# Kernel tuning notes

Measured on AMD Instinct MI355X. Metric: run time of the kernel, lower is better.

The kernel has to match this reference:

```python
import jax, jax.numpy as jnp
import numpy as np

N = 8192       # nodes
NFEAT = 512    # input features
NHID = 64      # per-head hidden
NHEADS = 4
NCLASS = 40
ALPHA = 0.2    # leaky_relu negative slope
EDGE_P = 0.01  # adjacency density (plus self-loops)


def setup_inputs() -> dict:
    key = jax.random.key(0)
    k = jax.random.split(key, 6)
    x = jax.random.normal(k[0], (N, NFEAT), dtype=jnp.float32)
    adj = jax.random.bernoulli(k[1], EDGE_P, (N, N))
    adj = adj | jnp.eye(N, dtype=bool)  # self-loops so no row is fully masked
    W1 = jax.random.normal(k[2], (NHEADS, NFEAT, NHID), dtype=jnp.float32) * 0.05
    a1 = jax.random.normal(k[3], (NHEADS, 2 * NHID), dtype=jnp.float32) * 0.05
    Wo = jax.random.normal(k[4], (NHEADS * NHID, NCLASS), dtype=jnp.float32) * 0.05
    ao = jax.random.normal(k[5], (2 * NCLASS,), dtype=jnp.float32) * 0.05
    return {"x": x, "adj": adj, "W1": W1, "a1": a1, "Wo": Wo, "ao": ao}


def _gat_head(h, adj, W, a, concat):
    # GAT attention head: e_ij = leaky_relu(a1 . Wh_i + a2 . Wh_j), masked by adj
    Wh = h @ W                      # [N, F']
    Fp = W.shape[1]
    f_src = Wh @ a[:Fp]             # [N]
    f_dst = Wh @ a[Fp:]             # [N]
    e = jax.nn.leaky_relu(f_src[:, None] + f_dst[None, :], negative_slope=ALPHA)
    e = jnp.where(adj, e, jnp.float32(-9e15))
    att = jax.nn.softmax(e, axis=1)  # [N, N]
    out = att @ Wh                   # [N, F']
    return jax.nn.elu(out) if concat else out


def reference(x, adj, W1, a1, Wo, ao):
    # dropout is identity in eval mode
    heads = [_gat_head(x, adj, W1[i], a1[i], concat=True) for i in range(NHEADS)]
    x1 = jnp.concatenate(heads, axis=1)            # [N, NHEADS*NHID]
    out = jax.nn.elu(_gat_head(x1, adj, Wo, ao, concat=False))  # [N, NCLASS]
    return jax.nn.log_softmax(out, axis=1)
```

## Files before the change

kernel.cpp:

```cpp
#include <hip/hip_runtime.h>
#include <hip/hip_bf16.h>


#define N_NODES 8192
#define STRIDE  192

typedef _Float16 f16x8 __attribute__((ext_vector_type(8)));
typedef float    f32x4 __attribute__((ext_vector_type(4)));

__global__ __launch_bounds__(256) void prep_k(
    const float* __restrict__ x, const unsigned char* __restrict__ adjb,
    const float* __restrict__ W1, const float* __restrict__ Wo,
    _Float16* __restrict__ xh, _Float16* __restrict__ B1t, _Float16* __restrict__ B2t,
    int* __restrict__ nbr, int* __restrict__ deg)
{
    const int b = blockIdx.x;
    const int tid = threadIdx.x;
    if (b < N_NODES) {
        __shared__ int cnt;
        if (tid == 0) cnt = 0;
        __syncthreads();
        const bool bytewise = (adjb[8193] == 1);
        if (bytewise) {
            const uint4* p = (const uint4*)(adjb + (size_t)b * N_NODES);
            #pragma unroll
            for (int q = 0; q < 2; ++q) {
                const int idx = tid + 256 * q;
                uint4 v = p[idx];
                unsigned int ws_[4] = {v.x, v.y, v.z, v.w};
                #pragma unroll
                for (int wj = 0; wj < 4; ++wj) {
                    unsigned int u = ws_[wj];
                    if (u) {
                        #pragma unroll
                        for (int by = 0; by < 4; ++by) {
                            if ((u >> (8 * by)) & 0xFFu) {
                                int c = idx * 16 + wj * 4 + by;
                                int pos = atomicAdd(&cnt, 1);
                                if (pos < STRIDE) nbr[(size_t)b * STRIDE + pos] = c;
                            }
                        }
                    }
                }
            }
        } else {
            const int4* p = (const int4*)((const int*)(const void*)adjb + (size_t)b * N_NODES);
            #pragma unroll
            for (int q = 0; q < 8; ++q) {
                const int idx = tid + 256 * q;
                int4 v = p[idx];
                if (v.x) { int pos = atomicAdd(&cnt, 1); if (pos < STRIDE) nbr[(size_t)b * STRIDE + pos] = idx * 4 + 0; }
                if (v.y) { int pos = atomicAdd(&cnt, 1); if (pos < STRIDE) nbr[(size_t)b * STRIDE + pos] = idx * 4 + 1; }
                if (v.z) { int pos = atomicAdd(&cnt, 1); if (pos < STRIDE) nbr[(size_t)b * STRIDE + pos] = idx * 4 + 2; }
                if (v.w) { int pos = atomicAdd(&cnt, 1); if (pos < STRIDE) nbr[(size_t)b * STRIDE + pos] = idx * 4 + 3; }
            }
        }
        __syncthreads();
        if (tid == 0) deg[b] = (cnt < STRIDE) ? cnt : STRIDE;
    } else if (b < N_NODES + 2048) {
        const size_t base = (size_t)(b - N_NODES) * 2048 + (size_t)tid * 8;
        float4 v0 = *(const float4*)(x + base);
        float4 v1 = *(const float4*)(x + base + 4);
        f16x8 o;
        o[0] = (_Float16)v0.x; o[1] = (_Float16)v0.y; o[2] = (_Float16)v0.z; o[3] = (_Float16)v0.w;
        o[4] = (_Float16)v1.x; o[5] = (_Float16)v1.y; o[6] = (_Float16)v1.z; o[7] = (_Float16)v1.w;
        *(f16x8*)(xh + base) = o;
    } else if (b < N_NODES + 2048 + 64) {
        const int e0 = (b - (N_NODES + 2048)) * 2048 + tid * 8;
        const int n = e0 >> 9;
        const int k0 = e0 & 511;
        const int h = n >> 6, j = n & 63;
        const float* src = W1 + (size_t)h * 32768 + j;
        f16x8 o;
        #pragma unroll
        for (int r = 0; r < 8; ++r) o[r] = (_Float16)src[(size_t)(k0 + r) * 64];
        *(f16x8*)(B1t + e0) = o;
    } else {
        const int e = (b - (N_NODES + 2048 + 64)) * 256 + tid;
        const int n = e >> 8, k = e & 255;
        B2t[e] = (n < 40) ? (_Float16)Wo[(size_t)k * 40 + n] : (_Float16)0.0f;
    }
}

template<int BM, int BN, int BK, int WR, int WC, int KTOT>
__global__ __launch_bounds__(256) void gemm_k(
    const _Float16* __restrict__ A, const _Float16* __restrict__ Bt,
    _Float16* __restrict__ C, int NTOT)
{
    constexpr int WTM = BM / WR;
    constexpr int WTN = BN / WC;
    constexpr int MFR = WTM / 16;
    constexpr int NFR = WTN / 16;
    constexpr int CPR = BK / 8;
    static_assert(CPR == 8, "swizzle assumes BK=64");
    __shared__ _Float16 As[BM * BK];
    __shared__ _Float16 Bs[BN * BK];
    const int tid = threadIdx.x;
    const int lane = tid & 63;
    const int wv = tid >> 6;
    const int wr = wv / WC, wc = wv % WC;
    const long brow = (long)blockIdx.x * BM;
    const long bcol = (long)blockIdx.y * BN;
    f32x4 acc[MFR][NFR] = {};

    for (int k0 = 0; k0 < KTOT; k0 += BK) {
        #pragma unroll
        for (int q = 0; q < (BM * BK / 8) / 256; ++q) {
            int cid = tid + 256 * q;
            int row = cid / CPR, cc = cid % CPR;
            f16x8 v = *(const f16x8*)(A + (brow + row) * KTOT + k0 + cc * 8);
            *(f16x8*)(As + row * BK + ((cc ^ (row & 7)) & (CPR - 1)) * 8) = v;
        }
        #pragma unroll
        for (int q = 0; q < (BN * BK / 8) / 256; ++q) {
            int cid = tid + 256 * q;
            int row = cid / CPR, cc = cid % CPR;
            f16x8 v = *(const f16x8*)(Bt + (bcol + row) * KTOT + k0 + cc * 8);
            *(f16x8*)(Bs + row * BK + ((cc ^ (row & 7)) & (CPR - 1)) * 8) = v;
        }
        __syncthreads();
        #pragma unroll
        for (int kk = 0; kk < BK; kk += 32) {
            f16x8 af[MFR], bf[NFR];
            #pragma unroll
            for (int m = 0; m < MFR; ++m) {
                int row = wr * WTM + m * 16 + (lane & 15);
                int cc = (kk >> 3) + (lane >> 4);
                af[m] = *(const f16x8*)(As + row * BK + ((cc ^ (row & 7)) & (CPR - 1)) * 8);
            }
            #pragma unroll
            for (int n = 0; n < NFR; ++n) {
                int row = wc * WTN + n * 16 + (lane & 15);
                int cc = (kk >> 3) + (lane >> 4);
                bf[n] = *(const f16x8*)(Bs + row * BK + ((cc ^ (row & 7)) & (CPR - 1)) * 8);
            }
            #pragma unroll
            for (int m = 0; m < MFR; ++m)
                #pragma unroll
                for (int n = 0; n < NFR; ++n)
                    acc[m][n] = __builtin_amdgcn_mfma_f32_16x16x32_f16(af[m], bf[n], acc[m][n], 0, 0, 0);
        }
        __syncthreads();
    }
    #pragma unroll
    for (int m = 0; m < MFR; ++m)
        #pragma unroll
        for (int n = 0; n < NFR; ++n)
            #pragma unroll
            for (int r = 0; r < 4; ++r) {
                long row = brow + wr * WTM + m * 16 + (lane >> 4) * 4 + r;
                long col = bcol + wc * WTN + n * 16 + (lane & 15);
                C[row * NTOT + col] = (_Float16)acc[m][n][r];
            }
}

__global__ __launch_bounds__(256) void fsd1_k(
    const _Float16* __restrict__ Wh, const float* __restrict__ a1,
    float* __restrict__ fs, float* __restrict__ fd)
{
    const int i = blockIdx.x;
    const int h = threadIdx.x >> 6, j = threadIdx.x & 63;
    float v = (float)Wh[(size_t)i * 256 + h * 64 + j];
    float s = v * a1[h * 128 + j];
    float d = v * a1[h * 128 + 64 + j];
    #pragma unroll
    for (int o = 32; o; o >>= 1) { s += __shfl_xor(s, o); d += __shfl_xor(d, o); }
    if (j == 0) { fs[h * N_NODES + i] = s; fd[h * N_NODES + i] = d; }
}

__global__ __launch_bounds__(256) void agg1_k(
    const int* __restrict__ nbr, const int* __restrict__ deg,
    const _Float16* __restrict__ Wh, const float* __restrict__ fs,
    const float* __restrict__ fd, _Float16* __restrict__ x1)
{
    const int i = blockIdx.x;
    const int h = threadIdx.x >> 6, lane = threadIdx.x & 63;
    __shared__ float satt[4][STRIDE];
    __shared__ int scol[STRIDE];
    const int d = deg[i];
    const float fsi = fs[h * N_NODES + i];
    float e0 = -1e30f, e1 = -1e30f, e2 = -1e30f;
    int c0 = 0, c1 = 0, c2 = 0;
    if (lane < d)       { c0 = nbr[(size_t)i * STRIDE + lane];       float t = fsi + fd[h * N_NODES + c0]; e0 = t > 0.f ? t : 0.2f * t; }
    if (lane + 64 < d)  { c1 = nbr[(size_t)i * STRIDE + lane + 64];  float t = fsi + fd[h * N_NODES + c1]; e1 = t > 0.f ? t : 0.2f * t; }
    if (lane + 128 < d) { c2 = nbr[(size_t)i * STRIDE + lane + 128]; float t = fsi + fd[h * N_NODES + c2]; e2 = t > 0.f ? t : 0.2f * t; }
    float mx = fmaxf(e0, fmaxf(e1, e2));
    #pragma unroll
    for (int o = 32; o; o >>= 1) mx = fmaxf(mx, __shfl_xor(mx, o));
    float w0 = (lane < d)       ? __expf(e0 - mx) : 0.f;
    float w1 = (lane + 64 < d)  ? __expf(e1 - mx) : 0.f;
    float w2 = (lane + 128 < d) ? __expf(e2 - mx) : 0.f;
    float s = w0 + w1 + w2;
    #pragma unroll
    for (int o = 32; o; o >>= 1) s += __shfl_xor(s, o);
    const float inv = 1.f / s;
    if (lane < d)       satt[h][lane] = w0 * inv;
    if (lane + 64 < d)  satt[h][lane + 64] = w1 * inv;
    if (lane + 128 < d) satt[h][lane + 128] = w2 * inv;
    if (h == 0) {
        if (lane < d)       scol[lane] = c0;
        if (lane + 64 < d)  scol[lane + 64] = c1;
        if (lane + 128 < d) scol[lane + 128] = c2;
    }
    __syncthreads();
    const _Float16* wp = Wh + h * 64 + lane;
    float a0 = 0.f, a1_ = 0.f, a2 = 0.f, a3 = 0.f, a4 = 0.f, a5 = 0.f, a6 = 0.f, a7 = 0.f;
    int t = 0;
    for (; t + 8 <= d; t += 8) {
        int s0 = scol[t], s1 = scol[t+1], s2 = scol[t+2], s3 = scol[t+3];
        int s4 = scol[t+4], s5 = scol[t+5], s6 = scol[t+6], s7 = scol[t+7];
        float g0 = (float)wp[(size_t)s0 * 256]; float g1 = (float)wp[(size_t)s1 * 256];
        float g2 = (float)wp[(size_t)s2 * 256]; float g3 = (float)wp[(size_t)s3 * 256];
        float g4 = (float)wp[(size_t)s4 * 256]; float g5 = (float)wp[(size_t)s5 * 256];
        float g6 = (float)wp[(size_t)s6 * 256]; float g7 = (float)wp[(size_t)s7 * 256];
        a0 += satt[h][t]   * g0; a1_ += satt[h][t+1] * g1;
        a2 += satt[h][t+2] * g2; a3 += satt[h][t+3] * g3;
        a4 += satt[h][t+4] * g4; a5 += satt[h][t+5] * g5;
        a6 += satt[h][t+6] * g6; a7 += satt[h][t+7] * g7;
    }
    for (; t < d; ++t) a0 += satt[h][t] * (float)wp[(size_t)scol[t] * 256];
    float acc = ((a0 + a1_) + (a2 + a3)) + ((a4 + a5) + (a6 + a7));
    float o = acc > 0.f ? acc : expm1f(acc);
    x1[(size_t)i * 256 + h * 64 + lane] = (_Float16)o;
}

__global__ __launch_bounds__(256) void fsd2_k(
    const _Float16* __restrict__ Who, const float* __restrict__ ao,
    float* __restrict__ fso, float* __restrict__ fdo)
{
    const int wv = threadIdx.x >> 6, lane = threadIdx.x & 63;
    const int i = blockIdx.x * 4 + wv;
    float v = (lane < 40) ? (float)Who[(size_t)i * 64 + lane] : 0.f;
    float s = (lane < 40) ? v * ao[lane] : 0.f;
    float d = (lane < 40) ? v * ao[40 + lane] : 0.f;
    #pragma unroll
    for (int o = 32; o; o >>= 1) { s += __shfl_xor(s, o); d += __shfl_xor(d, o); }
    if (lane == 0) { fso[i] = s; fdo[i] = d; }
}

__global__ __launch_bounds__(256) void agg2_k(
    const int* __restrict__ nbr, const int* __restrict__ deg,
    const _Float16* __restrict__ Who, const float* __restrict__ fso,
    const float* __restrict__ fdo, float* __restrict__ out)
{
    const int wv = threadIdx.x >> 6, lane = threadIdx.x & 63;
    const int i = blockIdx.x * 4 + wv;
    __shared__ float satt[4][STRIDE];
    __shared__ int scol[4][STRIDE];
    const int d = deg[i];
    const float fsi = fso[i];
    float e0 = -1e30f, e1 = -1e30f, e2 = -1e30f;
    int c0 = 0, c1 = 0, c2 = 0;
    if (lane < d)       { c0 = nbr[(size_t)i * STRIDE + lane];       float t = fsi + fdo[c0]; e0 = t > 0.f ? t : 0.2f * t; }
    if (lane + 64 < d)  { c1 = nbr[(size_t)i * STRIDE + lane + 64];  float t = fsi + fdo[c1]; e1 = t > 0.f ? t : 0.2f * t; }
    if (lane + 128 < d) { c2 = nbr[(size_t)i * STRIDE + lane + 128]; float t = fsi + fdo[c2]; e2 = t > 0.f ? t : 0.2f * t; }
    float mx = fmaxf(e0, fmaxf(e1, e2));
    #pragma unroll
    for (int o = 32; o; o >>= 1) mx = fmaxf(mx, __shfl_xor(mx, o));
    float w0 = (lane < d)       ? __expf(e0 - mx) : 0.f;
    float w1 = (lane + 64 < d)  ? __expf(e1 - mx) : 0.f;
    float w2 = (lane + 128 < d) ? __expf(e2 - mx) : 0.f;
    float s = w0 + w1 + w2;
    #pragma unroll
    for (int o = 32; o; o >>= 1) s += __shfl_xor(s, o);
    const float inv = 1.f / s;
    if (lane < d)       { satt[wv][lane] = w0 * inv;       scol[wv][lane] = c0; }
    if (lane + 64 < d)  { satt[wv][lane + 64] = w1 * inv;  scol[wv][lane + 64] = c1; }
    if (lane + 128 < d) { satt[wv][lane + 128] = w2 * inv; scol[wv][lane + 128] = c2; }
    __syncthreads();
    float a0 = 0.f, a1_ = 0.f, a2 = 0.f, a3 = 0.f, a4 = 0.f, a5 = 0.f, a6 = 0.f, a7 = 0.f;
    int t = 0;
    for (; t + 8 <= d; t += 8) {
        int s0 = scol[wv][t],   s1 = scol[wv][t+1], s2 = scol[wv][t+2], s3 = scol[wv][t+3];
        int s4 = scol[wv][t+4], s5 = scol[wv][t+5], s6 = scol[wv][t+6], s7 = scol[wv][t+7];
        float g0 = (float)Who[(size_t)s0 * 64 + lane]; float g1 = (float)Who[(size_t)s1 * 64 + lane];
        float g2 = (float)Who[(size_t)s2 * 64 + lane]; float g3 = (float)Who[(size_t)s3 * 64 + lane];
        float g4 = (float)Who[(size_t)s4 * 64 + lane]; float g5 = (float)Who[(size_t)s5 * 64 + lane];
        float g6 = (float)Who[(size_t)s6 * 64 + lane]; float g7 = (float)Who[(size_t)s7 * 64 + lane];
        a0 += satt[wv][t]   * g0; a1_ += satt[wv][t+1] * g1;
        a2 += satt[wv][t+2] * g2; a3 += satt[wv][t+3] * g3;
        a4 += satt[wv][t+4] * g4; a5 += satt[wv][t+5] * g5;
        a6 += satt[wv][t+6] * g6; a7 += satt[wv][t+7] * g7;
    }
    for (; t < d; ++t) a0 += satt[wv][t] * (float)Who[(size_t)scol[wv][t] * 64 + lane];
    float acc = ((a0 + a1_) + (a2 + a3)) + ((a4 + a5) + (a6 + a7));
    float v = acc > 0.f ? acc : expm1f(acc);
    float vm = (lane < 40) ? v : -1e30f;
    #pragma unroll
    for (int o = 32; o; o >>= 1) vm = fmaxf(vm, __shfl_xor(vm, o));
    float ex = (lane < 40) ? __expf(v - vm) : 0.f;
    #pragma unroll
    for (int o = 32; o; o >>= 1) ex += __shfl_xor(ex, o);
    if (lane < 40) out[(size_t)i * 40 + lane] = v - vm - __logf(ex);
}

extern "C" void kernel_launch(void* const* d_in, const int* in_sizes, int n_in,
                              void* d_out, int out_size, void* d_ws, size_t ws_size,
                              hipStream_t stream) {
    (void)in_sizes; (void)n_in; (void)out_size; (void)ws_size;
    const float* x = (const float*)d_in[0];
    const unsigned char* adjb = (const unsigned char*)d_in[1];
    const float* W1 = (const float*)d_in[2];
    const float* a1 = (const float*)d_in[3];
    const float* Wo = (const float*)d_in[4];
    const float* ao = (const float*)d_in[5];
    float* out = (float*)d_out;

    char* w = (char*)d_ws;
    size_t off = 0;
    auto alloc = [&](size_t bytes) -> void* {
        off = (off + 255) & ~(size_t)255;
        void* p = w + off; off += bytes; return p;
    };
    _Float16* xh  = (_Float16*)alloc((size_t)N_NODES * 512 * 2);
    _Float16* B1t = (_Float16*)alloc(256 * 512 * 2);
    _Float16* B2t = (_Float16*)alloc(64 * 256 * 2);
    _Float16* Wh  = (_Float16*)alloc((size_t)N_NODES * 256 * 2);
    _Float16* x1  = (_Float16*)alloc((size_t)N_NODES * 256 * 2);
    _Float16* Who = (_Float16*)alloc((size_t)N_NODES * 64 * 2);
    float* fs1 = (float*)alloc(4 * N_NODES * 4);
    float* fd1 = (float*)alloc(4 * N_NODES * 4);
    float* fso = (float*)alloc(N_NODES * 4);
    float* fdo = (float*)alloc(N_NODES * 4);
    int* nbr = (int*)alloc((size_t)N_NODES * STRIDE * 4);
    int* deg = (int*)alloc(N_NODES * 4);

    prep_k<<<dim3(N_NODES + 2048 + 64 + 64), dim3(256), 0, stream>>>(x, adjb, W1, Wo, xh, B1t, B2t, nbr, deg);
    gemm_k<64, 64, 64, 2, 2, 512><<<dim3(128, 4), dim3(256), 0, stream>>>(xh, B1t, Wh, 256);
    fsd1_k<<<dim3(N_NODES), dim3(256), 0, stream>>>(Wh, a1, fs1, fd1);
    agg1_k<<<dim3(N_NODES), dim3(256), 0, stream>>>(nbr, deg, Wh, fs1, fd1, x1);
    gemm_k<32, 64, 64, 2, 2, 256><<<dim3(256, 1), dim3(256), 0, stream>>>(x1, B2t, Who, 64);
    fsd2_k<<<dim3(N_NODES / 4), dim3(256), 0, stream>>>(Who, ao, fso, fdo);
    agg2_k<<<dim3(N_NODES / 4), dim3(256), 0, stream>>>(nbr, deg, Who, fso, fdo, out);
}
```

Baseline: 452.9 us.

## Fuse fp32-to-fp16 conversion and attention score projections into GEMM kernels

Removes the separate x-to-fp16 conversion pass by having the first GEMM load fp32 rows and convert them while staging into shared memory. The f_src/f_dst dot products, previously computed by two standalone kernels, are now done in the GEMM epilogues from the fp32 accumulators, reduced with shuffles and a small shared-memory buffer. This cuts two kernel launches and the round trips of the fp16 x copy and the Wh/Who re-reads. The cost is twice the bytes loaded per A tile in the first GEMM and a longer epilogue. The scores now come from fp32 accumulators rather than fp16-rounded values.

```diff
diff --git a/kernel.cpp b/kernel.cpp
--- a/kernel.cpp
+++ b/kernel.cpp
@@ -9,9 +9,9 @@
 typedef float    f32x4 __attribute__((ext_vector_type(4)));
 
 __global__ __launch_bounds__(256) void prep_k(
-    const float* __restrict__ x, const unsigned char* __restrict__ adjb,
+    const unsigned char* __restrict__ adjb,
     const float* __restrict__ W1, const float* __restrict__ Wo,
-    _Float16* __restrict__ xh, _Float16* __restrict__ B1t, _Float16* __restrict__ B2t,
+    _Float16* __restrict__ B1t, _Float16* __restrict__ B2t,
     int* __restrict__ nbr, int* __restrict__ deg)
 {
     const int b = blockIdx.x;
@@ -57,16 +57,8 @@
         }
         __syncthreads();
         if (tid == 0) deg[b] = (cnt < STRIDE) ? cnt : STRIDE;
-    } else if (b < N_NODES + 2048) {
-        const size_t base = (size_t)(b - N_NODES) * 2048 + (size_t)tid * 8;
-        float4 v0 = *(const float4*)(x + base);
-        float4 v1 = *(const float4*)(x + base + 4);
-        f16x8 o;
-        o[0] = (_Float16)v0.x; o[1] = (_Float16)v0.y; o[2] = (_Float16)v0.z; o[3] = (_Float16)v0.w;
-        o[4] = (_Float16)v1.x; o[5] = (_Float16)v1.y; o[6] = (_Float16)v1.z; o[7] = (_Float16)v1.w;
-        *(f16x8*)(xh + base) = o;
-    } else if (b < N_NODES + 2048 + 64) {
-        const int e0 = (b - (N_NODES + 2048)) * 2048 + tid * 8;
+    } else if (b < N_NODES + 64) {
+        const int e0 = (b - N_NODES) * 2048 + tid * 8;
         const int n = e0 >> 9;
         const int k0 = e0 & 511;
         const int h = n >> 6, j = n & 63;
@@ -76,16 +68,17 @@
         for (int r = 0; r < 8; ++r) o[r] = (_Float16)src[(size_t)(k0 + r) * 64];
         *(f16x8*)(B1t + e0) = o;
     } else {
-        const int e = (b - (N_NODES + 2048 + 64)) * 256 + tid;
+        const int e = (b - (N_NODES + 64)) * 256 + tid;
         const int n = e >> 8, k = e & 255;
         B2t[e] = (n < 40) ? (_Float16)Wo[(size_t)k * 40 + n] : (_Float16)0.0f;
     }
 }
 
-template<int BM, int BN, int BK, int WR, int WC, int KTOT>
+template<int BM, int BN, int BK, int WR, int WC, int KTOT, bool SRC32, int MODE>
 __global__ __launch_bounds__(256) void gemm_k(
-    const _Float16* __restrict__ A, const _Float16* __restrict__ Bt,
-    _Float16* __restrict__ C, int NTOT)
+    const void* __restrict__ Ap, const _Float16* __restrict__ Bt,
+    _Float16* __restrict__ C, const float* __restrict__ av,
+    float* __restrict__ fs, float* __restrict__ fd, int NTOT)
 {
     constexpr int WTM = BM / WR;
     constexpr int WTN = BN / WC;
@@ -108,7 +101,16 @@
         for (int q = 0; q < (BM * BK / 8) / 256; ++q) {
             int cid = tid + 256 * q;
             int row = cid / CPR, cc = cid % CPR;
-            f16x8 v = *(const f16x8*)(A + (brow + row) * KTOT + k0 + cc * 8);
+            f16x8 v;
+            if constexpr (SRC32) {
+                const float* A32 = (const float*)Ap;
+                float4 v0 = *(const float4*)(A32 + (brow + row) * KTOT + k0 + cc * 8);
+                float4 v1 = *(const float4*)(A32 + (brow + row) * KTOT + k0 + cc * 8 + 4);
+                v[0] = (_Float16)v0.x; v[1] = (_Float16)v0.y; v[2] = (_Float16)v0.z; v[3] = (_Float16)v0.w;
+                v[4] = (_Float16)v1.x; v[5] = (_Float16)v1.y; v[6] = (_Float16)v1.z; v[7] = (_Float16)v1.w;
+            } else {
+                v = *(const f16x8*)((const _Float16*)Ap + (brow + row) * KTOT + k0 + cc * 8);
+            }
             *(f16x8*)(As + row * BK + ((cc ^ (row & 7)) & (CPR - 1)) * 8) = v;
         }
         #pragma unroll
@@ -152,20 +154,42 @@
                 long col = bcol + wc * WTN + n * 16 + (lane & 15);
                 C[row * NTOT + col] = (_Float16)acc[m][n][r];
             }
-}
-
-__global__ __launch_bounds__(256) void fsd1_k(
-    const _Float16* __restrict__ Wh, const float* __restrict__ a1,
-    float* __restrict__ fs, float* __restrict__ fd)
-{
-    const int i = blockIdx.x;
-    const int h = threadIdx.x >> 6, j = threadIdx.x & 63;
-    float v = (float)Wh[(size_t)i * 256 + h * 64 + j];
-    float s = v * a1[h * 128 + j];
-    float d = v * a1[h * 128 + 64 + j];
-    #pragma unroll
-    for (int o = 32; o; o >>= 1) { s += __shfl_xor(s, o); d += __shfl_xor(d, o); }
-    if (j == 0) { fs[h * N_NODES + i] = s; fd[h * N_NODES + i] = d; }
+    if constexpr (MODE > 0) {
+        constexpr int AVN = (MODE == 1) ? 64 : 40;
+        const float* asrc = (MODE == 1) ? av + blockIdx.y * 128 : av;
+        const float* adst = (MODE == 1) ? av + blockIdx.y * 128 + 64 : av + 40;
+        float* fsb = (MODE == 1) ? fs + blockIdx.y * N_NODES + brow : fs + brow;
+        float* fdb = (MODE == 1) ? fd + blockIdx.y * N_NODES + brow : fd + brow;
+        __shared__ float sred[WC][2][BM];
+        float as_[NFR], ad_[NFR];
+        #pragma unroll
+        for (int n = 0; n < NFR; ++n) {
+            int j = wc * WTN + n * 16 + (lane & 15);
+            as_[n] = (j < AVN) ? asrc[j] : 0.f;
+            ad_[n] = (j < AVN) ? adst[j] : 0.f;
+        }
+        #pragma unroll
+        for (int m = 0; m < MFR; ++m)
+            #pragma unroll
+            for (int r = 0; r < 4; ++r) {
+                float vfs = 0.f, vfd = 0.f;
+                #pragma unroll
+                for (int n = 0; n < NFR; ++n) { vfs += acc[m][n][r] * as_[n]; vfd += acc[m][n][r] * ad_[n]; }
+                #pragma unroll
+                for (int o = 1; o < 16; o <<= 1) { vfs += __shfl_xor(vfs, o); vfd += __shfl_xor(vfd, o); }
+                if ((lane & 15) == 0) {
+                    int row = wr * WTM + m * 16 + (lane >> 4) * 4 + r;
+                    sred[wc][0][row] = vfs; sred[wc][1][row] = vfd;
+                }
+            }
+        __syncthreads();
+        if (tid < BM) {
+            float s = 0.f, dd = 0.f;
+            #pragma unroll
+            for (int w2 = 0; w2 < WC; ++w2) { s += sred[w2][0][tid]; dd += sred[w2][1][tid]; }
+            fsb[tid] = s; fdb[tid] = dd;
+        }
+    }
 }
 
 __global__ __launch_bounds__(256) void agg1_k(
@@ -222,20 +246,6 @@
     float acc = ((a0 + a1_) + (a2 + a3)) + ((a4 + a5) + (a6 + a7));
     float o = acc > 0.f ? acc : expm1f(acc);
     x1[(size_t)i * 256 + h * 64 + lane] = (_Float16)o;
-}
-
-__global__ __launch_bounds__(256) void fsd2_k(
-    const _Float16* __restrict__ Who, const float* __restrict__ ao,
-    float* __restrict__ fso, float* __restrict__ fdo)
-{
-    const int wv = threadIdx.x >> 6, lane = threadIdx.x & 63;
-    const int i = blockIdx.x * 4 + wv;
-    float v = (lane < 40) ? (float)Who[(size_t)i * 64 + lane] : 0.f;
-    float s = (lane < 40) ? v * ao[lane] : 0.f;
-    float d = (lane < 40) ? v * ao[40 + lane] : 0.f;
-    #pragma unroll
-    for (int o = 32; o; o >>= 1) { s += __shfl_xor(s, o); d += __shfl_xor(d, o); }
-    if (lane == 0) { fso[i] = s; fdo[i] = d; }
 }
 
 __global__ __launch_bounds__(256) void agg2_k(
@@ -312,7 +322,6 @@
         off = (off + 255) & ~(size_t)255;
         void* p = w + off; off += bytes; return p;
     };
-    _Float16* xh  = (_Float16*)alloc((size_t)N_NODES * 512 * 2);
     _Float16* B1t = (_Float16*)alloc(256 * 512 * 2);
     _Float16* B2t = (_Float16*)alloc(64 * 256 * 2);
     _Float16* Wh  = (_Float16*)alloc((size_t)N_NODES * 256 * 2);
@@ -325,11 +334,11 @@
     int* nbr = (int*)alloc((size_t)N_NODES * STRIDE * 4);
     int* deg = (int*)alloc(N_NODES * 4);
 
-    prep_k<<<dim3(N_NODES + 2048 + 64 + 64), dim3(256), 0, stream>>>(x, adjb, W1, Wo, xh, B1t, B2t, nbr, deg);
-    gemm_k<64, 64, 64, 2, 2, 512><<<dim3(128, 4), dim3(256), 0, stream>>>(xh, B1t, Wh, 256);
-    fsd1_k<<<dim3(N_NODES), dim3(256), 0, stream>>>(Wh, a1, fs1, fd1);
+    prep_k<<<dim3(N_NODES + 64 + 64), dim3(256), 0, stream>>>(adjb, W1, Wo, B1t, B2t, nbr, deg);
+    gemm_k<64, 64, 64, 2, 2, 512, true, 1><<<dim3(128, 4), dim3(256), 0, stream>>>(
+        x, B1t, Wh, a1, fs1, fd1, 256);
     agg1_k<<<dim3(N_NODES), dim3(256), 0, stream>>>(nbr, deg, Wh, fs1, fd1, x1);
-    gemm_k<32, 64, 64, 2, 2, 256><<<dim3(256, 1), dim3(256), 0, stream>>>(x1, B2t, Who, 64);
-    fsd2_k<<<dim3(N_NODES / 4), dim3(256), 0, stream>>>(Who, ao, fso, fdo);
+    gemm_k<32, 64, 64, 2, 2, 256, false, 2><<<dim3(256, 1), dim3(256), 0, stream>>>(
+        x1, B2t, Who, ao, fso, fdo, 64);
     agg2_k<<<dim3(N_NODES / 4), dim3(256), 0, stream>>>(nbr, deg, Who, fso, fdo, out);
 }
```

New measurement: 445.2 us. Within noise of the previous version (-1.7%).
